# Performance work log

Hardware: AMD Instinct MI355X
Metric: run time of the kernel (lower is better)

Reference implementation:

```python
import jax, jax.numpy as jnp
import numpy as np

B, L, D, H = 2, 4096, 1024, 8
DK = D // H   # per-head key dim = 128
DV = D // H   # per-head value dim = 128
K_CONV = 4
CHUNK = 64
EPS = 1e-6


def _rmsnorm(x, w):
    return x * jax.lax.rsqrt(jnp.mean(x * x, axis=-1, keepdims=True) + EPS) * w


def _l2norm(x):
    return x * jax.lax.rsqrt(jnp.sum(x * x, axis=-1, keepdims=True) + EPS)


def _short_conv(x, w):
    # causal depthwise conv (FLA ShortConvolution) + silu. x: [B,L,C], w: [C,K]
    Kc = w.shape[-1]
    Ln = x.shape[1]
    xp = jnp.pad(x, ((0, 0), (Kc - 1, 0), (0, 0)))
    y = xp[:, 0:Ln, :] * w[:, 0]
    for i in range(1, Kc):
        y = y + xp[:, i:i + Ln, :] * w[:, i]
    return jax.nn.silu(y)


def _delta_chunkwise(q, k, v, beta, chunk=CHUNK):
    # q,k: [B,H,L,DK], v: [B,H,L,DV], beta: [B,H,L]
    Bb, Hh, Ll, Dk = q.shape
    Dv = v.shape[-1]
    q = q * (Dk ** -0.5)
    nC = Ll // chunk  # L divisible by chunk here, no padding needed
    qc = q.reshape(Bb, Hh, nC, chunk, Dk).transpose(2, 0, 1, 3, 4)
    kc = k.reshape(Bb, Hh, nC, chunk, Dk).transpose(2, 0, 1, 3, 4)
    vc = v.reshape(Bb, Hh, nC, chunk, Dv).transpose(2, 0, 1, 3, 4)
    bc = beta.reshape(Bb, Hh, nC, chunk).transpose(2, 0, 1, 3)
    eye = jnp.eye(chunk, dtype=q.dtype)
    causal = jnp.tril(jnp.ones((chunk, chunk), dtype=q.dtype))

    def step(S, inp):
        q_c, k_c, v_c, b_c = inp
        kk = jnp.einsum('bhik,bhjk->bhij', k_c, k_c)
        A = eye + jnp.tril(b_c[..., :, None] * kk, k=-1)
        A_inv = jax.lax.linalg.triangular_solve(
            A, jnp.broadcast_to(eye, A.shape), left_side=True, lower=True,
            transpose_a=False, conjugate_a=False, unit_diagonal=False)
        w_ = jnp.einsum('bhij,bhjk->bhik', A_inv, k_c * b_c[..., None])
        u_ = jnp.einsum('bhij,bhjv->bhiv', A_inv, v_c * b_c[..., None])
        v_new = u_ - jnp.einsum('bhik,bhkv->bhiv', w_, S)
        qk = jnp.einsum('bhik,bhjk->bhij', q_c, k_c)
        o = jnp.einsum('bhik,bhkv->bhiv', q_c, S) + jnp.einsum('bhij,bhjv->bhiv', qk * causal, v_new)
        S_new = S + jnp.einsum('bhik,bhiv->bhkv', k_c, v_new)
        return S_new, o

    S0 = jnp.zeros((Bb, Hh, Dk, Dv), dtype=q.dtype)
    S_f, outs = jax.lax.scan(step, S0, (qc, kc, vc, bc))
    out = outs.transpose(1, 2, 0, 3, 4).reshape(Bb, Hh, Ll, Dv)
    return out, S_f


def setup_inputs() -> dict:
    key = jax.random.key(0)
    ks = jax.random.split(key, 9)
    s = 0.02
    return {
        'x': jax.random.normal(ks[0], (B, L, D), jnp.float32),
        'norm_w': jnp.ones((D,), jnp.float32),
        'Wq': jax.random.normal(ks[1], (D, D), jnp.float32) * s,
        'Wk': jax.random.normal(ks[2], (D, D), jnp.float32) * s,
        'Wv': jax.random.normal(ks[3], (D, D), jnp.float32) * s,
        'Wb': jax.random.normal(ks[4], (D, H), jnp.float32) * s,
        'conv_q': jax.random.normal(ks[5], (D, K_CONV), jnp.float32) * 0.3,
        'conv_k': jax.random.normal(ks[6], (D, K_CONV), jnp.float32) * 0.3,
        'conv_v': jax.random.normal(ks[7], (D, K_CONV), jnp.float32) * 0.3,
        'o_norm_w': jnp.ones((DV,), jnp.float32),
        'Wo': jax.random.normal(ks[8], (D, D), jnp.float32) * s,
    }


def reference(x, norm_w, Wq, Wk, Wv, Wb, conv_q, conv_k, conv_v, o_norm_w, Wo):
    h = _rmsnorm(x, norm_w)
    q = _short_conv(h @ Wq, conv_q)
    k = _short_conv(h @ Wk, conv_k)
    v = _short_conv(h @ Wv, conv_v)
    beta = jax.nn.sigmoid(h @ Wb)                      # [B,L,H]
    qh = q.reshape(B, L, H, DK).transpose(0, 2, 1, 3)  # [B,H,L,DK]
    kh = k.reshape(B, L, H, DK).transpose(0, 2, 1, 3)
    vh = v.reshape(B, L, H, DV).transpose(0, 2, 1, 3)
    qh = _l2norm(jax.nn.silu(qh))  # qk_activation=silu, qk_norm=l2
    kh = _l2norm(jax.nn.silu(kh))
    bh = beta.transpose(0, 2, 1)   # [B,H,L]
    o, _ = _delta_chunkwise(qh, kh, vh, bh)
    o = o.transpose(0, 2, 1, 3)    # [B,L,H,DV]
    o = _rmsnorm(o, o_norm_w)      # per-head output RMSNorm
    return x + o.reshape(B, L, D) @ Wo
```

## Files before the change

kernel.cpp:

```cpp
#include <hip/hip_runtime.h>
#include <hip/hip_bf16.h>

#define B_ 2
#define L_ 4096
#define D_ 1024
#define H_ 8
#define DK_ 128
#define NR_ (B_*L_)
#define NC_ 64
#define CS_ 64

typedef __attribute__((ext_vector_type(8))) short short8;
typedef __attribute__((ext_vector_type(4))) float f32x4;

__device__ __forceinline__ float sigmf(float x){ return 1.0f/(1.0f+__expf(-x)); }
__device__ __forceinline__ float siluf(float x){ return x/(1.0f+__expf(-x)); }
__device__ __forceinline__ unsigned short f2bf(float f){
  __hip_bfloat16 h = __float2bfloat16(f);
  return *reinterpret_cast<unsigned short*>(&h);
}
__device__ __forceinline__ void gll16(const void* g, void* l){
  __builtin_amdgcn_global_load_lds((const __attribute__((address_space(1))) void*)g,
      (__attribute__((address_space(3))) void*)l, 16, 0, 0);
}

__global__ __launch_bounds__(256) void rmsnorm_kernel(const float* __restrict__ x,
    const float* __restrict__ w, float* __restrict__ h, unsigned short* __restrict__ hb){
  int n = blockIdx.x; int t = threadIdx.x;
  float4 v = ((const float4*)(x + (size_t)n*D_))[t];
  float ss = v.x*v.x + v.y*v.y + v.z*v.z + v.w*v.w;
  #pragma unroll
  for (int m=32;m>0;m>>=1) ss += __shfl_xor(ss, m, 64);
  __shared__ float red[4];
  if ((t&63)==0) red[t>>6] = ss;
  __syncthreads();
  ss = red[0]+red[1]+red[2]+red[3];
  float rs = rsqrtf(ss*(1.0f/D_) + 1e-6f);
  float4 wv = ((const float4*)w)[t];
  float4 o; o.x=v.x*rs*wv.x; o.y=v.y*rs*wv.y; o.z=v.z*rs*wv.z; o.w=v.w*rs*wv.w;
  ((float4*)(h + (size_t)n*D_))[t] = o;
  ushort4 ob4; ob4.x=f2bf(o.x); ob4.y=f2bf(o.y); ob4.z=f2bf(o.z); ob4.w=f2bf(o.w);
  ((ushort4*)(hb + (size_t)n*D_))[t] = ob4;
}

__global__ __launch_bounds__(256) void transpose_bf16_kernel(const float* __restrict__ W,
    unsigned short* __restrict__ Wt){
  __shared__ float tile[64][65];
  int bi = blockIdx.y, bj = blockIdx.x;
  int tx = threadIdx.x & 63, tg = threadIdx.x >> 6;
  #pragma unroll
  for (int i=0;i<16;i++){
    int r = tg*16 + i;
    tile[r][tx] = W[(size_t)(bi*64 + r)*D_ + bj*64 + tx];
  }
  __syncthreads();
  #pragma unroll
  for (int i=0;i<16;i++){
    int r = tg*16 + i;
    Wt[(size_t)(bj*64 + r)*D_ + bi*64 + tx] = f2bf(tile[tx][r]);
  }
}

__global__ __launch_bounds__(256) void gemm_bf16(const unsigned short* __restrict__ A,
    const unsigned short* __restrict__ Bt, const float* __restrict__ R,
    float* __restrict__ C, int N, int K){
  __shared__ __align__(16) unsigned short Al[4096];
  __shared__ __align__(16) unsigned short Bl[4096];
  int t = threadIdx.x, w = t>>6, l = t&63;
  int wm = w&1, wn = w>>1;
  int row0 = blockIdx.y*128, col0 = blockIdx.x*128;
  int lr = l&15, lk = l>>4;
  const unsigned short* ga0 = A  + (size_t)(row0 + w*16     + lr)*K + lk*8;
  const unsigned short* ga1 = A  + (size_t)(row0 + (w+4)*16 + lr)*K + lk*8;
  const unsigned short* gb0 = Bt + (size_t)(col0 + w*16     + lr)*K + lk*8;
  const unsigned short* gb1 = Bt + (size_t)(col0 + (w+4)*16 + lr)*K + lk*8;
  unsigned short* la0 = &Al[(w*64 + l)*8];
  unsigned short* la1 = &Al[((w+4)*64 + l)*8];
  unsigned short* lb0 = &Bl[(w*64 + l)*8];
  unsigned short* lb1 = &Bl[((w+4)*64 + l)*8];
  f32x4 acc[4][4];
  #pragma unroll
  for (int i=0;i<4;i++)
    #pragma unroll
    for (int j=0;j<4;j++) acc[i][j] = (f32x4){0.f,0.f,0.f,0.f};
  for (int k0=0;k0<K;k0+=32){
    gll16(ga0 + k0, la0);
    gll16(ga1 + k0, la1);
    gll16(gb0 + k0, lb0);
    gll16(gb1 + k0, lb1);
    __syncthreads();
    short8 af[4], bfr[4];
    #pragma unroll
    for (int i=0;i<4;i++) af[i]  = *(const short8*)&Al[((wm*4+i)*64 + l)*8];
    #pragma unroll
    for (int j=0;j<4;j++) bfr[j] = *(const short8*)&Bl[((wn*4+j)*64 + l)*8];
    #pragma unroll
    for (int i=0;i<4;i++)
      #pragma unroll
      for (int j=0;j<4;j++)
        acc[i][j] = __builtin_amdgcn_mfma_f32_16x16x32_bf16(af[i], bfr[j], acc[i][j], 0,0,0);
    __syncthreads();
  }
  int orow = row0 + wm*64 + (l>>4)*4;
  int ocol = col0 + wn*64 + (l&15);
  #pragma unroll
  for (int i=0;i<4;i++){
    #pragma unroll
    for (int j=0;j<4;j++){
      #pragma unroll
      for (int r=0;r<4;r++){
        size_t idx = (size_t)(orow + i*16 + r)*N + ocol + j*16;
        float res = R ? R[idx] : 0.0f;
        C[idx] = acc[i][j][r] + res;
      }
    }
  }
}

__global__ __launch_bounds__(256) void beta_kernel(const float* __restrict__ h,
    const float* __restrict__ Wb, float* __restrict__ beta){
  int n = blockIdx.x, t = threadIdx.x;
  const float* hr = h + (size_t)n*D_;
  float p[8] = {};
  for (int kx=t; kx<D_; kx+=256){
    float hv = hr[kx];
    const float* wr = Wb + (size_t)kx*H_;
    #pragma unroll
    for (int j=0;j<8;j++) p[j] += hv*wr[j];
  }
  #pragma unroll
  for (int m=32;m>0;m>>=1){
    #pragma unroll
    for (int j=0;j<8;j++) p[j] += __shfl_xor(p[j], m, 64);
  }
  __shared__ float red[4][8];
  if ((t&63)==0){
    #pragma unroll
    for (int j=0;j<8;j++) red[t>>6][j] = p[j];
  }
  __syncthreads();
  if (t < 8){
    float s = red[0][t]+red[1][t]+red[2][t]+red[3][t];
    beta[(size_t)n*H_ + t] = sigmf(s);
  }
}

__global__ __launch_bounds__(256) void conv_silu_kernel(const float* __restrict__ in,
    const float* __restrict__ w, float* __restrict__ out, int ld){
  size_t idx = (size_t)blockIdx.x*256 + threadIdx.x;
  int c = (int)(idx & (D_-1));
  int n = (int)(idx >> 10);
  int l = n & (L_-1);
  const float* src = in + (size_t)n*ld + c;
  float4 wv = ((const float4*)w)[c];
  float acc = wv.w * src[0];
  if (l >= 1) acc += wv.z * src[-ld];
  if (l >= 2) acc += wv.y * src[-2*ld];
  if (l >= 3) acc += wv.x * src[-3*ld];
  out[(size_t)n*D_ + c] = siluf(acc);
}

__global__ __launch_bounds__(256) void conv_silu_l2norm_kernel(const float* __restrict__ in,
    const float* __restrict__ w, float* __restrict__ outf, unsigned short* __restrict__ ob,
    float scale, int ld){
  int n = blockIdx.x, t = threadIdx.x;
  int c0 = t*4;
  int l = n & (L_-1);
  const float* src = in + (size_t)n*ld + c0;
  float4 x0 = *(const float4*)&src[0];
  float4 x1 = (l>=1) ? *(const float4*)&src[-ld]   : (float4){0,0,0,0};
  float4 x2 = (l>=2) ? *(const float4*)&src[-2*ld] : (float4){0,0,0,0};
  float4 x3 = (l>=3) ? *(const float4*)&src[-3*ld] : (float4){0,0,0,0};
  float4 w0 = ((const float4*)w)[c0+0];
  float4 w1 = ((const float4*)w)[c0+1];
  float4 w2 = ((const float4*)w)[c0+2];
  float4 w3 = ((const float4*)w)[c0+3];
  float4 u;
  u.x = siluf(w0.w*x0.x + w0.z*x1.x + w0.y*x2.x + w0.x*x3.x);
  u.y = siluf(w1.w*x0.y + w1.z*x1.y + w1.y*x2.y + w1.x*x3.y);
  u.z = siluf(w2.w*x0.z + w2.z*x1.z + w2.y*x2.z + w2.x*x3.z);
  u.w = siluf(w3.w*x0.w + w3.z*x1.w + w3.y*x2.w + w3.x*x3.w);
  u.x = siluf(u.x); u.y = siluf(u.y); u.z = siluf(u.z); u.w = siluf(u.w);
  float ss = u.x*u.x+u.y*u.y+u.z*u.z+u.w*u.w;
  #pragma unroll
  for (int m=16;m>0;m>>=1) ss += __shfl_xor(ss, m, 64);
  float rs = rsqrtf(ss + 1e-6f) * scale;
  u.x*=rs; u.y*=rs; u.z*=rs; u.w*=rs;
  ((float4*)(outf + (size_t)n*D_))[t] = u;
  if (ob){
    ushort4 r4; r4.x=f2bf(u.x); r4.y=f2bf(u.y); r4.z=f2bf(u.z); r4.w=f2bf(u.w);
    ((ushort4*)(ob + (size_t)n*D_))[t] = r4;
  }
}

__global__ __launch_bounds__(256) void chunk_local_kernel(
    const float* __restrict__ q, const float* __restrict__ k, const float* __restrict__ v,
    const float* __restrict__ beta, unsigned short* __restrict__ wneg_buf,
    float* __restrict__ u_buf, unsigned short* __restrict__ qk_buf,
    unsigned short* __restrict__ kt_buf){
  int ci = blockIdx.x, bh = blockIdx.y;
  int b = bh >> 3, hh = bh & 7;
  int n0 = b*L_ + ci*CS_;
  int cbase = hh*DK_;
  int cid = bh*NC_ + ci;
  __shared__ float Ks[64][132];
  __shared__ float Als[64*68];
  __shared__ float rowW[144];
  __shared__ float rowU[144];
  __shared__ float bs[64];
  int t = threadIdx.x;
  {
    int r = t >> 2, c0 = (t & 3)*32;
    const float* kr = k + (size_t)(n0+r)*D_ + cbase + c0;
    #pragma unroll
    for (int m=0;m<32;m+=4) *(float4*)&Ks[r][c0+m] = *(const float4*)&kr[m];
  }
  if (t < 64) bs[t] = beta[(size_t)(n0+t)*H_ + hh];
  __syncthreads();
  int ti = t >> 4, tj = t & 15;
  {
    float cc[4][4] = {};
    #pragma unroll 2
    for (int d=0; d<128; d+=4){
      float4 ar[4], br[4];
      #pragma unroll
      for (int r2=0;r2<4;r2++) ar[r2] = *(const float4*)&Ks[ti+16*r2][d];
      #pragma unroll
      for (int s2=0;s2<4;s2++) br[s2] = *(const float4*)&Ks[tj+16*s2][d];
      #pragma unroll
      for (int r2=0;r2<4;r2++){
        #pragma unroll
        for (int s2=0;s2<4;s2++){
          cc[r2][s2] += ar[r2].x*br[s2].x + ar[r2].y*br[s2].y
                      + ar[r2].z*br[s2].z + ar[r2].w*br[s2].w;
        }
      }
    }
    #pragma unroll
    for (int r2=0;r2<4;r2++){
      #pragma unroll
      for (int s2=0;s2<4;s2++){
        int i2 = ti + 16*r2, j2 = tj + 16*s2;
        Als[i2*68 + j2] = (j2 < i2) ? bs[i2]*cc[r2][s2] : 0.0f;
      }
    }
  }
  __syncthreads();
  int i = t >> 2, part = t & 3, ds = part*32, dp = part*36;
  float wreg[32], ureg[32];
  {
    float bi = bs[i];
    const float* vr = v + (size_t)(n0+i)*D_ + cbase + ds;
    #pragma unroll
    for (int m=0;m<32;m++) wreg[m] = bi * Ks[i][ds+m];
    #pragma unroll
    for (int m=0;m<32;m+=4){
      float4 vv = *(const float4*)&vr[m];
      ureg[m+0]=bi*vv.x; ureg[m+1]=bi*vv.y; ureg[m+2]=bi*vv.z; ureg[m+3]=bi*vv.w;
    }
  }
  for (int j=0;j<63;j++){
    if (i == j){
      #pragma unroll
      for (int m=0;m<32;m++){ rowW[dp+m]=wreg[m]; rowU[dp+m]=ureg[m]; }
    }
    __syncthreads();
    if (i > j){
      float aj = Als[i*68 + j];
      #pragma unroll
      for (int m=0;m<32;m++){ wreg[m] -= aj*rowW[dp+m]; ureg[m] -= aj*rowU[dp+m]; }
    }
    __syncthreads();
  }
  {
    unsigned short* wd = wneg_buf + (size_t)cid*(64*128) + (size_t)i*128 + ds;
    float* ud = u_buf + (size_t)cid*(64*128) + (size_t)i*128 + ds;
    #pragma unroll
    for (int m=0;m<32;m+=4){
      ushort4 f; f.x=f2bf(-wreg[m]); f.y=f2bf(-wreg[m+1]); f.z=f2bf(-wreg[m+2]); f.w=f2bf(-wreg[m+3]);
      *(ushort4*)&wd[m] = f;
      float4 g; g.x=ureg[m]; g.y=ureg[m+1]; g.z=ureg[m+2]; g.w=ureg[m+3];
      *(float4*)&ud[m] = g;
    }
  }
  __syncthreads();
  {
    const float* qbase = q + (size_t)n0*D_ + cbase;
    float cc[4][4] = {};
    #pragma unroll 2
    for (int d=0; d<128; d+=4){
      float4 ar[4], br[4];
      #pragma unroll
      for (int r2=0;r2<4;r2++) ar[r2] = *(const float4*)&qbase[(size_t)(ti+16*r2)*D_ + d];
      #pragma unroll
      for (int s2=0;s2<4;s2++) br[s2] = *(const float4*)&Ks[tj+16*s2][d];
      #pragma unroll
      for (int r2=0;r2<4;r2++){
        #pragma unroll
        for (int s2=0;s2<4;s2++){
          cc[r2][s2] += ar[r2].x*br[s2].x + ar[r2].y*br[s2].y
                      + ar[r2].z*br[s2].z + ar[r2].w*br[s2].w;
        }
      }
    }
    unsigned short* qkd = qk_buf + (size_t)cid*4096;
    #pragma unroll
    for (int r2=0;r2<4;r2++){
      #pragma unroll
      for (int s2=0;s2<4;s2++){
        int i2 = ti+16*r2, j2 = tj+16*s2;
        qkd[i2*64 + j2] = (j2 <= i2) ? f2bf(cc[r2][s2]) : (unsigned short)0;
      }
    }
  }
  {
    unsigned short* ktd = kt_buf + (size_t)cid*(64*128);
    for (int idx = t; idx < 8192; idx += 256){
      int d = idx >> 6, i2 = idx & 63;
      ktd[idx] = f2bf(Ks[i2][d]);
    }
  }
}

__global__ __launch_bounds__(512) void seq_kernel(
    const unsigned short* __restrict__ wneg_buf, const float* __restrict__ u_buf,
    const unsigned short* __restrict__ kt_buf, const unsigned short* __restrict__ qk_buf,
    const unsigned short* __restrict__ qbh, float* __restrict__ o_buf){
  int bid = blockIdx.x;
  int bh = bid & 15, cg = bid >> 4;
  int b = bh >> 3, hh = bh & 7;
  int cbase = hh*DK_;
  int t = threadIdx.x;
  int w = t >> 6, l = t & 63, g = l >> 4, lr = l & 15;
  int mt = w >> 1, nt = w & 1;
  int ct = w >> 2, dtp = (w & 3)*2;

  __shared__ __align__(16) unsigned short Wl[2][8192];
  __shared__ __align__(16) unsigned short Ql[2][8192];
  __shared__ __align__(16) unsigned short Ktl[2][8192];
  __shared__ __align__(16) unsigned short qkl[2][4096];
  __shared__ __align__(16) float  Ul[2][2048];
  __shared__ __align__(16) unsigned short Stl[2][32*136];
  __shared__ __align__(16) unsigned short vTl[32*72];

  f32x4 Sacc[2];
  Sacc[0] = (f32x4){0.f,0.f,0.f,0.f};
  Sacc[1] = (f32x4){0.f,0.f,0.f,0.f};

  for (int z=t; z<2*32*136; z+=512) ((unsigned short*)Stl)[z] = 0;

  size_t cid0 = (size_t)bh*NC_;
  const unsigned short* wb_  = wneg_buf + cid0*8192;
  const unsigned short* ktb_ = kt_buf  + cid0*8192;
  const unsigned short* qkb_ = qk_buf  + cid0*4096;
  const float*          ub_  = u_buf   + cid0*8192;
  const unsigned short* qb_  = qbh + (size_t)(b*L_)*D_ + cbase;

  int offW[2], offQ[2], offK[2];
  #pragma unroll
  for (int r=0;r<2;r++){
    int u = r*512 + t;
    int fm = u>>8, kq = (u>>6)&3, ll = u&63;
    offW[r] = (16*fm + (ll&15))*128 + kq*32 + (ll>>4)*8;
    offQ[r] = (16*fm + (ll&15))*D_  + kq*32 + (ll>>4)*8;
    int fn = u>>7, kqk = (u>>6)&1;
    offK[r] = (16*fn + (ll&15))*64 + kqk*32 + (ll>>4)*8;
  }
  int offQk, offU;
  {
    int u = t;
    int fm = u>>7, kq = (u>>6)&1, ll = u&63;
    offQk = (16*fm + (ll&15))*64 + kq*32 + (ll>>4)*8;
    offU  = (u>>3)*128 + cg*32 + (u&7)*4;
  }

  #define STAGE(BI, CI) do { \
    const unsigned short* wp  = wb_  + (size_t)(CI)*8192; \
    const unsigned short* kp  = ktb_ + (size_t)(CI)*8192; \
    const unsigned short* qkp = qkb_ + (size_t)(CI)*4096; \
    const float*          up  = ub_  + (size_t)(CI)*8192; \
    const unsigned short* qp  = qb_  + (size_t)(CI)*CS_*D_; \
    _Pragma("unroll") \
    for (int r=0;r<2;r++){ \
      gll16(wp + offW[r], &Wl[BI][(r*512+t)*8]); \
      gll16(qp + offQ[r], &Ql[BI][(r*512+t)*8]); \
      gll16(kp + offK[r], &Ktl[BI][(r*512+t)*8]); \
    } \
    gll16(qkp + offQk, &qkl[BI][t*8]); \
    gll16(up + offU, &Ul[BI][t*4]); \
  } while(0)

  STAGE(0, 0);
  asm volatile("s_waitcnt vmcnt(0) lgkmcnt(0)" ::: "memory");
  __builtin_amdgcn_s_barrier();
  __builtin_amdgcn_sched_barrier(0);

  int cur = 0;
  for (int ci=0; ci<NC_; ++ci){
    int cn = (ci+1 < NC_) ? ci+1 : ci;
    STAGE(cur^1, cn);

    f32x4 accV;
    #pragma unroll
    for (int r=0;r<4;r++) accV[r] = Ul[cur][(16*mt + 4*g + r)*32 + 16*nt + lr];
    #pragma unroll
    for (int kq=0;kq<4;kq++){
      short8 a  = *(const short8*)&Wl[cur][(mt*4+kq)*512 + l*8];
      short8 b0 = *(const short8*)&Stl[cur][(16*nt + lr)*136 + kq*32 + g*8];
      accV = __builtin_amdgcn_mfma_f32_16x16x32_bf16(a, b0, accV, 0,0,0);
    }
    #pragma unroll
    for (int r=0;r<4;r++)
      vTl[(16*nt + lr)*72 + 16*mt + 4*g + r] = f2bf(accV[r]);
    asm volatile("s_waitcnt lgkmcnt(0)" ::: "memory");
    __builtin_amdgcn_s_barrier();
    __builtin_amdgcn_sched_barrier(0);

    #pragma unroll
    for (int kq=0;kq<2;kq++){
      short8 aD = *(const short8*)&vTl[(16*ct + lr)*72 + kq*32 + g*8];
      short8 bD0 = *(const short8*)&Ktl[cur][((dtp+0)*2 + kq)*512 + l*8];
      short8 bD1 = *(const short8*)&Ktl[cur][((dtp+1)*2 + kq)*512 + l*8];
      Sacc[0] = __builtin_amdgcn_mfma_f32_16x16x32_bf16(aD, bD0, Sacc[0], 0,0,0);
      Sacc[1] = __builtin_amdgcn_mfma_f32_16x16x32_bf16(aD, bD1, Sacc[1], 0,0,0);
    }
    f32x4 accO = (f32x4){0.f,0.f,0.f,0.f};
    #pragma unroll
    for (int kq=0;kq<4;kq++){
      short8 a  = *(const short8*)&Ql[cur][(mt*4+kq)*512 + l*8];
      short8 b0 = *(const short8*)&Stl[cur][(16*nt + lr)*136 + kq*32 + g*8];
      accO = __builtin_amdgcn_mfma_f32_16x16x32_bf16(a, b0, accO, 0,0,0);
    }
    #pragma unroll
    for (int kq=0;kq<2;kq++){
      short8 a  = *(const short8*)&qkl[cur][(mt*2+kq)*512 + l*8];
      short8 b0 = *(const short8*)&vTl[(16*nt + lr)*72 + kq*32 + g*8];
      accO = __builtin_amdgcn_mfma_f32_16x16x32_bf16(a, b0, accO, 0,0,0);
    }
    #pragma unroll
    for (int j=0;j<2;j++){
      #pragma unroll
      for (int r=0;r<4;r++)
        Stl[cur^1][(16*ct + 4*g + r)*136 + 16*(dtp+j) + lr] = f2bf(Sacc[j][r]);
    }
    {
      int n0 = b*L_ + ci*CS_;
      #pragma unroll
      for (int r=0;r<4;r++)
        o_buf[(size_t)(n0 + 16*mt + 4*g + r)*D_ + cbase + cg*32 + 16*nt + lr] = accO[r];
    }
    asm volatile("s_waitcnt lgkmcnt(0)" ::: "memory");
    asm volatile("s_waitcnt vmcnt(4)" ::: "memory");
    __builtin_amdgcn_s_barrier();
    __builtin_amdgcn_sched_barrier(0);
    cur ^= 1;
  }
  #undef STAGE
}

__global__ __launch_bounds__(256) void head_rmsnorm_kernel(const float* __restrict__ o,
    const float* __restrict__ w, unsigned short* __restrict__ out){
  int n = blockIdx.x, t = threadIdx.x;
  float4 v = ((const float4*)(o + (size_t)n*D_))[t];
  float ss = v.x*v.x+v.y*v.y+v.z*v.z+v.w*v.w;
  #pragma unroll
  for (int m=16;m>0;m>>=1) ss += __shfl_xor(ss, m, 64);
  float rs = rsqrtf(ss*(1.0f/DK_) + 1e-6f);
  float4 wv = ((const float4*)w)[t & 31];
  float4 u; u.x=v.x*rs*wv.x; u.y=v.y*rs*wv.y; u.z=v.z*rs*wv.z; u.w=v.w*rs*wv.w;
  ushort4 r4; r4.x=f2bf(u.x); r4.y=f2bf(u.y); r4.z=f2bf(u.z); r4.w=f2bf(u.w);
  ((ushort4*)(out + (size_t)n*D_))[t] = r4;
}

extern "C" void kernel_launch(void* const* d_in, const int* in_sizes, int n_in,
                              void* d_out, int out_size, void* d_ws, size_t ws_size,
                              hipStream_t stream){
  const float* x      = (const float*)d_in[0];
  const float* norm_w = (const float*)d_in[1];
  const float* Wq     = (const float*)d_in[2];
  const float* Wk     = (const float*)d_in[3];
  const float* Wv     = (const float*)d_in[4];
  const float* Wb     = (const float*)d_in[5];
  const float* conv_q = (const float*)d_in[6];
  const float* conv_k = (const float*)d_in[7];
  const float* conv_v = (const float*)d_in[8];
  const float* onw    = (const float*)d_in[9];
  const float* Wo     = (const float*)d_in[10];
  float* out = (float*)d_out;

  const size_t NB = (size_t)NR_*D_;
  float* ws   = (float*)d_ws;
  float* h    = ws;
  float* qkv  = ws + NB;
  float* qb   = ws + 4*NB;
  float* kb   = ws + 5*NB;
  float* vb   = ws + 6*NB;
  float* betab= ws + 7*NB;
  unsigned short* wtq = (unsigned short*)(betab + 65536);
  unsigned short* wtk = wtq + (size_t)D_*D_;
  unsigned short* wtv = wtk + (size_t)D_*D_;
  unsigned short* wto = wtv + (size_t)D_*D_;
  unsigned short* hb  = (unsigned short*)qb;
  unsigned short* obb = (unsigned short*)h;
  unsigned short* qbh = (unsigned short*)(h + NB/2);
  unsigned short* wneg = (unsigned short*)qkv;
  unsigned short* ktb  = wneg + (size_t)8*1024*1024;
  unsigned short* qkbf = ktb  + (size_t)8*1024*1024;
  float*          ubuf = (float*)(qkbf + (size_t)4*1024*1024);

  rmsnorm_kernel<<<NR_, 256, 0, stream>>>(x, norm_w, h, hb);
  dim3 tg(16,16);
  transpose_bf16_kernel<<<tg, 256, 0, stream>>>(Wq, wtq);
  transpose_bf16_kernel<<<tg, 256, 0, stream>>>(Wk, wtk);
  transpose_bf16_kernel<<<tg, 256, 0, stream>>>(Wv, wtv);
  transpose_bf16_kernel<<<tg, 256, 0, stream>>>(Wo, wto);
  dim3 gq(3*D_/128, NR_/128);
  gemm_bf16<<<gq, 256, 0, stream>>>(hb, wtq, nullptr, qkv, 3*D_, D_);
  beta_kernel<<<NR_, 256, 0, stream>>>(h, Wb, betab);
  const float qscale = 0.08838834764831845f;
  conv_silu_l2norm_kernel<<<NR_, 256, 0, stream>>>(qkv,      conv_q, qb, qbh, qscale, 3*D_);
  conv_silu_l2norm_kernel<<<NR_, 256, 0, stream>>>(qkv + D_, conv_k, kb, nullptr, 1.0f, 3*D_);
  conv_silu_kernel<<<(int)(NB/256), 256, 0, stream>>>(qkv + 2*D_, conv_v, vb, 3*D_);
  chunk_local_kernel<<<dim3(NC_, 16), 256, 0, stream>>>(qb, kb, vb, betab,
      wneg, ubuf, qkbf, ktb);
  seq_kernel<<<64, 512, 0, stream>>>(wneg, ubuf, ktb, qkbf, qbh, vb);
  head_rmsnorm_kernel<<<NR_, 256, 0, stream>>>(vb, onw, obb);
  dim3 gg(D_/128, NR_/128);
  gemm_bf16<<<gg, 256, 0, stream>>>(obb, wto, x, out, D_, D_);
  (void)in_sizes; (void)n_in; (void)out_size; (void)ws_size;
}
```

Baseline: 688.6 us.

## Fuse beta projection into rmsnorm, batch weight transposes, double-buffer GEMM LDS

```diff
diff --git a/kernel.cpp b/kernel.cpp
--- a/kernel.cpp
+++ b/kernel.cpp
@@ -24,28 +24,63 @@
       (__attribute__((address_space(3))) void*)l, 16, 0, 0);
 }
 
-__global__ __launch_bounds__(256) void rmsnorm_kernel(const float* __restrict__ x,
-    const float* __restrict__ w, float* __restrict__ h, unsigned short* __restrict__ hb){
+__global__ __launch_bounds__(256) void rmsnorm_beta_kernel(const float* __restrict__ x,
+    const float* __restrict__ w, const float* __restrict__ Wb,
+    unsigned short* __restrict__ hb, float* __restrict__ beta){
   int n = blockIdx.x; int t = threadIdx.x;
   float4 v = ((const float4*)(x + (size_t)n*D_))[t];
   float ss = v.x*v.x + v.y*v.y + v.z*v.z + v.w*v.w;
   #pragma unroll
   for (int m=32;m>0;m>>=1) ss += __shfl_xor(ss, m, 64);
   __shared__ float red[4];
+  __shared__ float bred[4][8];
   if ((t&63)==0) red[t>>6] = ss;
   __syncthreads();
   ss = red[0]+red[1]+red[2]+red[3];
   float rs = rsqrtf(ss*(1.0f/D_) + 1e-6f);
   float4 wv = ((const float4*)w)[t];
   float4 o; o.x=v.x*rs*wv.x; o.y=v.y*rs*wv.y; o.z=v.z*rs*wv.z; o.w=v.w*rs*wv.w;
-  ((float4*)(h + (size_t)n*D_))[t] = o;
   ushort4 ob4; ob4.x=f2bf(o.x); ob4.y=f2bf(o.y); ob4.z=f2bf(o.z); ob4.w=f2bf(o.w);
   ((ushort4*)(hb + (size_t)n*D_))[t] = ob4;
-}
-
-__global__ __launch_bounds__(256) void transpose_bf16_kernel(const float* __restrict__ W,
+  float p[8];
+  {
+    const float* wb0 = Wb + (size_t)(t*4)*H_;
+    float4 a0 = *(const float4*)&wb0[0],  a1 = *(const float4*)&wb0[4];
+    float4 b0 = *(const float4*)&wb0[8],  b1 = *(const float4*)&wb0[12];
+    float4 c0 = *(const float4*)&wb0[16], c1 = *(const float4*)&wb0[20];
+    float4 d0 = *(const float4*)&wb0[24], d1 = *(const float4*)&wb0[28];
+    p[0]=o.x*a0.x+o.y*b0.x+o.z*c0.x+o.w*d0.x;
+    p[1]=o.x*a0.y+o.y*b0.y+o.z*c0.y+o.w*d0.y;
+    p[2]=o.x*a0.z+o.y*b0.z+o.z*c0.z+o.w*d0.z;
+    p[3]=o.x*a0.w+o.y*b0.w+o.z*c0.w+o.w*d0.w;
+    p[4]=o.x*a1.x+o.y*b1.x+o.z*c1.x+o.w*d1.x;
+    p[5]=o.x*a1.y+o.y*b1.y+o.z*c1.y+o.w*d1.y;
+    p[6]=o.x*a1.z+o.y*b1.z+o.z*c1.z+o.w*d1.z;
+    p[7]=o.x*a1.w+o.y*b1.w+o.z*c1.w+o.w*d1.w;
+  }
+  #pragma unroll
+  for (int m=32;m>0;m>>=1){
+    #pragma unroll
+    for (int j=0;j<8;j++) p[j] += __shfl_xor(p[j], m, 64);
+  }
+  if ((t&63)==0){
+    #pragma unroll
+    for (int j=0;j<8;j++) bred[t>>6][j] = p[j];
+  }
+  __syncthreads();
+  if (t < 8){
+    float s = bred[0][t]+bred[1][t]+bred[2][t]+bred[3][t];
+    beta[(size_t)n*H_ + t] = sigmf(s);
+  }
+}
+
+__global__ __launch_bounds__(256) void transpose4_bf16_kernel(const float* __restrict__ W0,
+    const float* __restrict__ W1, const float* __restrict__ W2, const float* __restrict__ W3,
     unsigned short* __restrict__ Wt){
   __shared__ float tile[64][65];
+  int z = blockIdx.z;
+  const float* W = (z==0)?W0:(z==1)?W1:(z==2)?W2:W3;
+  unsigned short* dst = Wt + (size_t)z*D_*D_;
   int bi = blockIdx.y, bj = blockIdx.x;
   int tx = threadIdx.x & 63, tg = threadIdx.x >> 6;
   #pragma unroll
@@ -57,15 +92,15 @@
   #pragma unroll
   for (int i=0;i<16;i++){
     int r = tg*16 + i;
-    Wt[(size_t)(bj*64 + r)*D_ + bi*64 + tx] = f2bf(tile[tx][r]);
+    dst[(size_t)(bj*64 + r)*D_ + bi*64 + tx] = f2bf(tile[tx][r]);
   }
 }
 
 __global__ __launch_bounds__(256) void gemm_bf16(const unsigned short* __restrict__ A,
     const unsigned short* __restrict__ Bt, const float* __restrict__ R,
     float* __restrict__ C, int N, int K){
-  __shared__ __align__(16) unsigned short Al[4096];
-  __shared__ __align__(16) unsigned short Bl[4096];
+  __shared__ __align__(16) unsigned short Al[2][4096];
+  __shared__ __align__(16) unsigned short Bl[2][4096];
   int t = threadIdx.x, w = t>>6, l = t&63;
   int wm = w&1, wn = w>>1;
   int row0 = blockIdx.y*128, col0 = blockIdx.x*128;
@@ -74,33 +109,43 @@
   const unsigned short* ga1 = A  + (size_t)(row0 + (w+4)*16 + lr)*K + lk*8;
   const unsigned short* gb0 = Bt + (size_t)(col0 + w*16     + lr)*K + lk*8;
   const unsigned short* gb1 = Bt + (size_t)(col0 + (w+4)*16 + lr)*K + lk*8;
-  unsigned short* la0 = &Al[(w*64 + l)*8];
-  unsigned short* la1 = &Al[((w+4)*64 + l)*8];
-  unsigned short* lb0 = &Bl[(w*64 + l)*8];
-  unsigned short* lb1 = &Bl[((w+4)*64 + l)*8];
+  int dA0 = (w*64 + l)*8, dA1 = ((w+4)*64 + l)*8;
   f32x4 acc[4][4];
   #pragma unroll
   for (int i=0;i<4;i++)
     #pragma unroll
     for (int j=0;j<4;j++) acc[i][j] = (f32x4){0.f,0.f,0.f,0.f};
-  for (int k0=0;k0<K;k0+=32){
-    gll16(ga0 + k0, la0);
-    gll16(ga1 + k0, la1);
-    gll16(gb0 + k0, lb0);
-    gll16(gb1 + k0, lb1);
-    __syncthreads();
+
+  #define GSTAGE(BI, KO) do { \
+    gll16(ga0 + (KO), &Al[BI][dA0]); \
+    gll16(ga1 + (KO), &Al[BI][dA1]); \
+    gll16(gb0 + (KO), &Bl[BI][dA0]); \
+    gll16(gb1 + (KO), &Bl[BI][dA1]); \
+  } while(0)
+
+  GSTAGE(0, 0);
+  asm volatile("s_waitcnt vmcnt(0)" ::: "memory");
+  __builtin_amdgcn_s_barrier();
+  __builtin_amdgcn_sched_barrier(0);
+  int nk = K >> 5, cur = 0;
+  for (int k=0; k<nk; ++k){
+    if (k+1 < nk) GSTAGE(cur^1, (k+1)*32);
     short8 af[4], bfr[4];
     #pragma unroll
-    for (int i=0;i<4;i++) af[i]  = *(const short8*)&Al[((wm*4+i)*64 + l)*8];
-    #pragma unroll
-    for (int j=0;j<4;j++) bfr[j] = *(const short8*)&Bl[((wn*4+j)*64 + l)*8];
+    for (int i=0;i<4;i++) af[i]  = *(const short8*)&Al[cur][((wm*4+i)*64 + l)*8];
+    #pragma unroll
+    for (int j=0;j<4;j++) bfr[j] = *(const short8*)&Bl[cur][((wn*4+j)*64 + l)*8];
     #pragma unroll
     for (int i=0;i<4;i++)
       #pragma unroll
       for (int j=0;j<4;j++)
         acc[i][j] = __builtin_amdgcn_mfma_f32_16x16x32_bf16(af[i], bfr[j], acc[i][j], 0,0,0);
-    __syncthreads();
-  }
+    asm volatile("s_waitcnt vmcnt(0)" ::: "memory");
+    __builtin_amdgcn_s_barrier();
+    __builtin_amdgcn_sched_barrier(0);
+    cur ^= 1;
+  }
+  #undef GSTAGE
   int orow = row0 + wm*64 + (l>>4)*4;
   int ocol = col0 + wn*64 + (l&15);
   #pragma unroll
@@ -114,34 +159,6 @@
         C[idx] = acc[i][j][r] + res;
       }
     }
-  }
-}
-
-__global__ __launch_bounds__(256) void beta_kernel(const float* __restrict__ h,
-    const float* __restrict__ Wb, float* __restrict__ beta){
-  int n = blockIdx.x, t = threadIdx.x;
-  const float* hr = h + (size_t)n*D_;
-  float p[8] = {};
-  for (int kx=t; kx<D_; kx+=256){
-    float hv = hr[kx];
-    const float* wr = Wb + (size_t)kx*H_;
-    #pragma unroll
-    for (int j=0;j<8;j++) p[j] += hv*wr[j];
-  }
-  #pragma unroll
-  for (int m=32;m>0;m>>=1){
-    #pragma unroll
-    for (int j=0;j<8;j++) p[j] += __shfl_xor(p[j], m, 64);
-  }
-  __shared__ float red[4][8];
-  if ((t&63)==0){
-    #pragma unroll
-    for (int j=0;j<8;j++) red[t>>6][j] = p[j];
-  }
-  __syncthreads();
-  if (t < 8){
-    float s = red[0][t]+red[1][t]+red[2][t]+red[3][t];
-    beta[(size_t)n*H_ + t] = sigmf(s);
   }
 }
 
@@ -497,9 +514,7 @@
   float* vb   = ws + 6*NB;
   float* betab= ws + 7*NB;
   unsigned short* wtq = (unsigned short*)(betab + 65536);
-  unsigned short* wtk = wtq + (size_t)D_*D_;
-  unsigned short* wtv = wtk + (size_t)D_*D_;
-  unsigned short* wto = wtv + (size_t)D_*D_;
+  unsigned short* wto = wtq + (size_t)3*D_*D_;
   unsigned short* hb  = (unsigned short*)qb;
   unsigned short* obb = (unsigned short*)h;
   unsigned short* qbh = (unsigned short*)(h + NB/2);
@@ -508,15 +523,10 @@
   unsigned short* qkbf = ktb  + (size_t)8*1024*1024;
   float*          ubuf = (float*)(qkbf + (size_t)4*1024*1024);
 
-  rmsnorm_kernel<<<NR_, 256, 0, stream>>>(x, norm_w, h, hb);
-  dim3 tg(16,16);
-  transpose_bf16_kernel<<<tg, 256, 0, stream>>>(Wq, wtq);
-  transpose_bf16_kernel<<<tg, 256, 0, stream>>>(Wk, wtk);
-  transpose_bf16_kernel<<<tg, 256, 0, stream>>>(Wv, wtv);
-  transpose_bf16_kernel<<<tg, 256, 0, stream>>>(Wo, wto);
+  rmsnorm_beta_kernel<<<NR_, 256, 0, stream>>>(x, norm_w, Wb, hb, betab);
+  transpose4_bf16_kernel<<<dim3(16,16,4), 256, 0, stream>>>(Wq, Wk, Wv, Wo, wtq);
   dim3 gq(3*D_/128, NR_/128);
   gemm_bf16<<<gq, 256, 0, stream>>>(hb, wtq, nullptr, qkv, 3*D_, D_);
-  beta_kernel<<<NR_, 256, 0, stream>>>(h, Wb, betab);
   const float qscale = 0.08838834764831845f;
   conv_silu_l2norm_kernel<<<NR_, 256, 0, stream>>>(qkv,      conv_q, qb, qbh, qscale, 3*D_);
   conv_silu_l2norm_kernel<<<NR_, 256, 0, stream>>>(qkv + D_, conv_k, kb, nullptr, 1.0f, 3*D_);
```

After: 682.5 us. No clear change (-0.9%).
